# Performance work log

Hardware: AMD Instinct MI355X
Metric: run time of the kernel (lower is better)

## Reference

```python
import jax, jax.numpy as jnp
import numpy as np

N_NODES = 16384
IN_DIM = 256
HEADS = 2
OUT_CH = 256  # per head
SLOPE = 0.2


def _gat_conv(x, edge_index, W, att_src, att_dst, bias):
    """PyG GATConv (v1), heads=2, concat=True, add_self_loops=True."""
    N = x.shape[0]
    loop = jnp.arange(N)
    src = jnp.concatenate([edge_index[0], loop])  # message sources j
    dst = jnp.concatenate([edge_index[1], loop])  # message targets i
    h = (x @ W.T).reshape(N, HEADS, OUT_CH)          # [N,H,C]
    a_src = (h * att_src).sum(-1)                    # [N,H]
    a_dst = (h * att_dst).sum(-1)                    # [N,H]
    e = jax.nn.leaky_relu(a_src[src] + a_dst[dst], SLOPE)  # [E,H]
    # segment softmax over incoming edges of each dst node
    m = jax.ops.segment_max(e, dst, num_segments=N)
    e = jnp.exp(e - m[dst])
    s = jax.ops.segment_sum(e, dst, num_segments=N)
    alpha = e / s[dst]                               # [E,H]
    out = jax.ops.segment_sum(alpha[:, :, None] * h[src], dst, num_segments=N)
    return out.reshape(N, HEADS * OUT_CH) + bias


def _safe_cdist(x):
    sq = (x * x).sum(-1)
    d2 = sq[:, None] + sq[None, :] - 2.0 * (x @ x.T)
    d2 = jnp.maximum(d2, 0.0)
    d = jnp.sqrt(jnp.where(d2 > 0, d2, 1.0))
    return jnp.where(d2 > 0, d, 0.0)


def _linear_init(k, out_f, in_f):
    b = 1.0 / np.sqrt(in_f)
    k1, k2 = jax.random.split(k)
    W = jax.random.uniform(k1, (out_f, in_f), minval=-b, maxval=b, dtype=jnp.float32)
    bias = jax.random.uniform(k2, (out_f,), minval=-b, maxval=b, dtype=jnp.float32)
    return W, bias


def setup_inputs() -> dict:
    key = jax.random.key(0)
    ks = jax.random.split(key, 12)
    x = jax.random.normal(ks[0], (N_NODES, IN_DIM), dtype=jnp.float32)
    edge_index = jax.random.randint(ks[1], (2, 524288), 0, N_NODES, dtype=jnp.int64)
    g = 1.0 / np.sqrt(IN_DIM)
    conv_W = jax.random.normal(ks[2], (HEADS * OUT_CH, IN_DIM), dtype=jnp.float32) * g
    att_src = jax.random.normal(ks[3], (HEADS, OUT_CH), dtype=jnp.float32) * g
    att_dst = jax.random.normal(ks[4], (HEADS, OUT_CH), dtype=jnp.float32) * g
    conv_b = jnp.zeros((HEADS * OUT_CH,), dtype=jnp.float32)
    Wa, ba = _linear_init(ks[5], 256, 512)
    W1, b1 = _linear_init(ks[6], 128, 256)
    W2, b2 = _linear_init(ks[7], 64, 128)
    W3, b3 = _linear_init(ks[8], 32, 64)
    W4, b4 = _linear_init(ks[9], 3, 32)
    return {"x": x, "edge_index": edge_index, "conv_W": conv_W,
            "att_src": att_src, "att_dst": att_dst, "conv_b": conv_b,
            "Wa": Wa, "ba": ba, "W1": W1, "b1": b1, "W2": W2, "b2": b2,
            "W3": W3, "b3": b3, "W4": W4, "b4": b4}


def reference(x, edge_index, conv_W, att_src, att_dst, conv_b,
              Wa, ba, W1, b1, W2, b2, W3, b3, W4, b4):
    h = _gat_conv(x, edge_index, conv_W, att_src, att_dst, conv_b)
    h = jax.nn.relu(h)                      # dropout = identity (eval)
    h = jax.nn.relu(h @ Wa.T + ba)
    h = jax.nn.relu(h @ W1.T + b1)
    h = jax.nn.relu(h @ W2.T + b2)
    h = jax.nn.relu(h @ W3.T + b3)
    h = h @ W4.T + b4                        # [N,3]
    return _safe_cdist(h)                    # [N,N]
```

## Files before the change

kernel.cpp:

```cpp
#include <hip/hip_runtime.h>
#include <math.h>
#include <stdint.h>

#define N_NODES 16384
#define E_EDGES 524288
#define E_TOT   (E_EDGES + N_NODES)
#define HDIM    512
#define SLOPE   0.2f

typedef unsigned short ushort_t;
typedef __attribute__((ext_vector_type(8))) short short8v;
typedef __attribute__((ext_vector_type(4))) float f32x4;

__device__ __forceinline__ unsigned short f2bf(float f) {
    unsigned u = __float_as_uint(f);
    return (unsigned short)((u + 0x7fffu + ((u >> 16) & 1u)) >> 16);
}
__device__ __forceinline__ float bf2f(unsigned short s) {
    return __uint_as_float(((unsigned)s) << 16);
}

#define GLOAD_LDS16(G, L)                                                               \
    __builtin_amdgcn_global_load_lds((const __attribute__((address_space(1))) unsigned int*)(G), \
                                     (__attribute__((address_space(3))) unsigned int*)(L), 16, 0, 0)

__global__ void detect_kernel(const void* __restrict__ ei, int* __restrict__ flag) {
    int t = threadIdx.x;
    int v = ((const int*)ei)[2 * t + 1];
    unsigned long long b = __ballot(v != 0);
    if (t == 0) *flag = (b == 0ULL) ? 1 : 0;
}

__device__ __forceinline__ int edge_val(const void* ei, int idx, int is64) {
    if (is64) return (int)((const long long*)ei)[idx];
    return ((const int*)ei)[idx];
}

__global__ __launch_bounds__(256) void count_kernel(const void* __restrict__ ei,
                                                    const int* __restrict__ flag,
                                                    int* __restrict__ deg) {
    int e = blockIdx.x * 256 + threadIdx.x;
    if (e >= E_TOT) return;
    int is64 = *flag;
    int dst = (e < E_EDGES) ? edge_val(ei, E_EDGES + e, is64) : (e - E_EDGES);
    atomicAdd(&deg[dst], 1);
}

__global__ __launch_bounds__(1024) void scan_kernel(const int* __restrict__ deg,
                                                    int* __restrict__ rowptr,
                                                    int* __restrict__ cursor) {
    __shared__ int ps[1024];
    int tid = threadIdx.x;
    int base = tid * 16;
    int loc[16];
    int s = 0;
#pragma unroll
    for (int i = 0; i < 16; ++i) { loc[i] = deg[base + i]; s += loc[i]; }
    ps[tid] = s;
    __syncthreads();
    for (int off = 1; off < 1024; off <<= 1) {
        int t = (tid >= off) ? ps[tid - off] : 0;
        __syncthreads();
        if (tid >= off) ps[tid] += t;
        __syncthreads();
    }
    int run = ps[tid] - s;
#pragma unroll
    for (int i = 0; i < 16; ++i) {
        rowptr[base + i] = run;
        cursor[base + i] = run;
        run += loc[i];
    }
    if (tid == 1023) rowptr[N_NODES] = run;
}

__global__ __launch_bounds__(256) void fill_kernel(const void* __restrict__ ei,
                                                   const int* __restrict__ flag,
                                                   int* __restrict__ cursor,
                                                   int* __restrict__ col) {
    int e = blockIdx.x * 256 + threadIdx.x;
    if (e >= E_TOT) return;
    int is64 = *flag;
    int src, dst;
    if (e < E_EDGES) {
        src = edge_val(ei, e, is64);
        dst = edge_val(ei, E_EDGES + e, is64);
    } else {
        src = dst = e - E_EDGES;
    }
    int slot = atomicAdd(&cursor[dst], 1);
    col[slot] = src;
}

template <bool BSTYLE>
__global__ __launch_bounds__(256) void split3_kernel(const float* __restrict__ src,
                                                     ushort_t* __restrict__ dst,
                                                     int kshift) {
    int idx = (blockIdx.x * 256 + threadIdx.x) * 4;
    int K = 1 << kshift;
    int row = idx >> kshift, c = idx & (K - 1);
    float4 v = *(const float4*)&src[idx];
    float f[4] = {v.x, v.y, v.z, v.w};
    ushort_t h4[4], l4[4];
#pragma unroll
    for (int q = 0; q < 4; ++q) {
        ushort_t hb = f2bf(f[q]);
        float r = f[q] - bf2f(hb);
        h4[q] = hb;
        l4[q] = f2bf(r);
    }
    size_t b = (size_t)row * (3 * (size_t)K) + c;
    *(ushort4*)&dst[b] = make_ushort4(h4[0], h4[1], h4[2], h4[3]);
    size_t off_hi2 = BSTYLE ? (size_t)(2 * K) : (size_t)K;
    size_t off_lo  = BSTYLE ? (size_t)K : (size_t)(2 * K);
    *(ushort4*)&dst[b + off_hi2] = make_ushort4(h4[0], h4[1], h4[2], h4[3]);
    *(ushort4*)&dst[b + off_lo]  = make_ushort4(l4[0], l4[1], l4[2], l4[3]);
}

template <int BN, bool RELU, bool BIAS>
__global__ __launch_bounds__(256) void mfma_gemm(const ushort_t* __restrict__ A,
                                                 const ushort_t* __restrict__ B,
                                                 const float* __restrict__ bias,
                                                 float* __restrict__ C,
                                                 int M, int N, int K) {
    constexpr int BM = 128, BK = 64;
    constexpr int ASLOTS = BM * BK / (256 * 8);
    constexpr int BSLOTS = BN * BK / (256 * 8);
    constexpr int BNF = BN / 32;
    __shared__ ushort_t As[BM * BK];
    __shared__ ushort_t Bs[BN * BK];

    int t = threadIdx.x;
    int bm0 = blockIdx.y * BM, bn0 = blockIdx.x * BN;

    size_t gA[ASLOTS]; int lA[ASLOTS];
#pragma unroll
    for (int s = 0; s < ASLOTS; ++s) {
        int lin = s * 256 + t;
        int row = lin >> 3, cs = (lin & 7) << 3;
        int lcol = cs ^ ((row & 7) << 3);
        gA[s] = (size_t)(bm0 + row) * K + lcol;
        lA[s] = (s * 256 + (t & ~63)) * 8;
    }
    size_t gB[BSLOTS]; int lB[BSLOTS];
#pragma unroll
    for (int s = 0; s < BSLOTS; ++s) {
        int lin = s * 256 + t;
        int row = lin >> 3, cs = (lin & 7) << 3;
        int lcol = cs ^ ((row & 7) << 3);
        gB[s] = (size_t)(bn0 + row) * K + lcol;
        lB[s] = (s * 256 + (t & ~63)) * 8;
    }

    int l = t & 63, w = t >> 6;
    int wm = w >> 1, wn = w & 1;
    int lr = l & 15, lk = l >> 4;

    f32x4 acc[4][BNF];
#pragma unroll
    for (int m = 0; m < 4; ++m)
#pragma unroll
        for (int n = 0; n < BNF; ++n) acc[m][n] = (f32x4){0.f, 0.f, 0.f, 0.f};

    for (int k0 = 0; k0 < K; k0 += BK) {
#pragma unroll
        for (int s = 0; s < ASLOTS; ++s) GLOAD_LDS16(A + gA[s] + k0, As + lA[s]);
#pragma unroll
        for (int s = 0; s < BSLOTS; ++s) GLOAD_LDS16(B + gB[s] + k0, Bs + lB[s]);
        __syncthreads();
#pragma unroll
        for (int ks = 0; ks < 2; ++ks) {
            short8v af[4], bfr[BNF];
#pragma unroll
            for (int m = 0; m < 4; ++m) {
                int row = wm * 64 + m * 16 + lr;
                int c = (ks * 32 + lk * 8) ^ ((row & 7) << 3);
                af[m] = *(const short8v*)&As[row * 64 + c];
            }
#pragma unroll
            for (int n = 0; n < BNF; ++n) {
                int row = wn * (BN / 2) + n * 16 + lr;
                int c = (ks * 32 + lk * 8) ^ ((row & 7) << 3);
                bfr[n] = *(const short8v*)&Bs[row * 64 + c];
            }
#pragma unroll
            for (int m = 0; m < 4; ++m)
#pragma unroll
                for (int n = 0; n < BNF; ++n)
                    acc[m][n] = __builtin_amdgcn_mfma_f32_16x16x32_bf16(af[m], bfr[n],
                                                                        acc[m][n], 0, 0, 0);
        }
        __syncthreads();
    }

#pragma unroll
    for (int m = 0; m < 4; ++m) {
        int row0 = bm0 + wm * 64 + m * 16 + lk * 4;
#pragma unroll
        for (int n = 0; n < BNF; ++n) {
            int cix = bn0 + wn * (BN / 2) + n * 16 + lr;
            float bv = BIAS ? bias[cix] : 0.f;
#pragma unroll
            for (int r = 0; r < 4; ++r) {
                float v = acc[m][n][r] + bv;
                if (RELU) v = fmaxf(v, 0.f);
                C[(size_t)(row0 + r) * N + cix] = v;
            }
        }
    }
}

__global__ __launch_bounds__(256) void attn_kernel(const float* __restrict__ h,
                                                   const float* __restrict__ att_src,
                                                   const float* __restrict__ att_dst,
                                                   float* __restrict__ a_src,
                                                   float* __restrict__ a_dst) {
    int n = blockIdx.x, tid = threadIdx.x;
    float h0 = h[(size_t)n * HDIM + tid];
    float h1 = h[(size_t)n * HDIM + 256 + tid];
    __shared__ float4 red[256];
    red[tid] = make_float4(h0 * att_src[tid], h1 * att_src[256 + tid],
                           h0 * att_dst[tid], h1 * att_dst[256 + tid]);
    __syncthreads();
    for (int off = 128; off > 0; off >>= 1) {
        if (tid < off) {
            float4 o = red[tid + off];
            float4 m = red[tid];
            m.x += o.x; m.y += o.y; m.z += o.z; m.w += o.w;
            red[tid] = m;
        }
        __syncthreads();
    }
    if (tid == 0) {
        float4 r = red[0];
        a_src[2 * n] = r.x; a_src[2 * n + 1] = r.y;
        a_dst[2 * n] = r.z; a_dst[2 * n + 1] = r.w;
    }
}

__device__ __forceinline__ float lrelu(float x) {
    return fmaxf(x, 0.f) + SLOPE * fminf(x, 0.f);
}

__global__ __launch_bounds__(256) void aggregate_kernel(const float* __restrict__ h,
                                                        const float* __restrict__ a_src,
                                                        const float* __restrict__ a_dst,
                                                        const int* __restrict__ rowptr,
                                                        const int* __restrict__ col,
                                                        const float* __restrict__ conv_b,
                                                        float* __restrict__ act0) {
    int n = blockIdx.x, tid = threadIdx.x;
    int rs = rowptr[n], re = rowptr[n + 1];
    float ad0 = a_dst[2 * n], ad1 = a_dst[2 * n + 1];
    __shared__ float r0[256], r1[256];

    float m0 = -1e30f, m1 = -1e30f;
    for (int k = rs + tid; k < re; k += 256) {
        int s = col[k];
        float e0 = lrelu(a_src[2 * s] + ad0);
        float e1 = lrelu(a_src[2 * s + 1] + ad1);
        m0 = fmaxf(m0, e0); m1 = fmaxf(m1, e1);
    }
    r0[tid] = m0; r1[tid] = m1;
    __syncthreads();
    for (int off = 128; off > 0; off >>= 1) {
        if (tid < off) {
            r0[tid] = fmaxf(r0[tid], r0[tid + off]);
            r1[tid] = fmaxf(r1[tid], r1[tid + off]);
        }
        __syncthreads();
    }
    float M0 = r0[0], M1 = r1[0];
    __syncthreads();

    float s0 = 0.f, s1 = 0.f;
    for (int k = rs + tid; k < re; k += 256) {
        int s = col[k];
        float e0 = lrelu(a_src[2 * s] + ad0);
        float e1 = lrelu(a_src[2 * s + 1] + ad1);
        s0 += expf(e0 - M0); s1 += expf(e1 - M1);
    }
    r0[tid] = s0; r1[tid] = s1;
    __syncthreads();
    for (int off = 128; off > 0; off >>= 1) {
        if (tid < off) {
            r0[tid] += r0[tid + off];
            r1[tid] += r1[tid + off];
        }
        __syncthreads();
    }
    float inv0 = 1.f / r0[0], inv1 = 1.f / r1[0];
    __syncthreads();

    __shared__ float al0[256], al1[256];
    __shared__ int sc[256];
    float acc0 = 0.f, acc1 = 0.f;
    for (int base = rs; base < re; base += 256) {
        int len = min(256, re - base);
        if (tid < len) {
            int s = col[base + tid];
            sc[tid] = s;
            float e0 = lrelu(a_src[2 * s] + ad0);
            float e1 = lrelu(a_src[2 * s + 1] + ad1);
            al0[tid] = expf(e0 - M0) * inv0;
            al1[tid] = expf(e1 - M1) * inv1;
        }
        __syncthreads();
        for (int kk = 0; kk < len; ++kk) {
            const float* hr = h + (size_t)sc[kk] * HDIM;
            acc0 = fmaf(al0[kk], hr[tid], acc0);
            acc1 = fmaf(al1[kk], hr[tid + 256], acc1);
        }
        __syncthreads();
    }
    act0[(size_t)n * HDIM + tid] = fmaxf(acc0 + conv_b[tid], 0.f);
    act0[(size_t)n * HDIM + 256 + tid] = fmaxf(acc1 + conv_b[tid + 256], 0.f);
}

__global__ __launch_bounds__(256) void mlp_tail_kernel(const float* __restrict__ act2,
                                                       const float* __restrict__ W2, const float* __restrict__ b2,
                                                       const float* __restrict__ W3, const float* __restrict__ b3,
                                                       const float* __restrict__ W4, const float* __restrict__ b4,
                                                       float* __restrict__ p) {
    __shared__ float w2[64][129];
    __shared__ float w3[32][65];
    __shared__ float w4[3][33];
    __shared__ float bb2[64], bb3[32], bb4[3];
    __shared__ float xb[4][128];
    __shared__ float yb[4][64];
    __shared__ float zb[4][32];
    int tid = threadIdx.x;
    for (int idx = tid; idx < 64 * 128; idx += 256) w2[idx >> 7][idx & 127] = W2[idx];
    for (int idx = tid; idx < 32 * 64; idx += 256) w3[idx >> 6][idx & 63] = W3[idx];
    for (int idx = tid; idx < 96; idx += 256) w4[idx / 32][idx % 32] = W4[idx];
    if (tid < 64) bb2[tid] = b2[tid];
    if (tid < 32) bb3[tid] = b3[tid];
    if (tid < 3) bb4[tid] = b4[tid];
    __syncthreads();

    int n0 = blockIdx.x * 64;
    int nl = tid >> 6, lane = tid & 63;
    for (int g = 0; g < 64; g += 4) {
        for (int lx = tid; lx < 512; lx += 256)
            xb[lx >> 7][lx & 127] = act2[(size_t)(n0 + g + (lx >> 7)) * 128 + (lx & 127)];
        __syncthreads();
        float y = bb2[lane];
#pragma unroll 8
        for (int j = 0; j < 128; ++j) y = fmaf(w2[lane][j], xb[nl][j], y);
        yb[nl][lane] = fmaxf(y, 0.f);
        __syncthreads();
        if (lane < 32) {
            float z = bb3[lane];
#pragma unroll 8
            for (int j = 0; j < 64; ++j) z = fmaf(w3[lane][j], yb[nl][j], z);
            zb[nl][lane] = fmaxf(z, 0.f);
        }
        __syncthreads();
        if (lane < 3) {
            float c = bb4[lane];
#pragma unroll
            for (int j = 0; j < 32; ++j) c = fmaf(w4[lane][j], zb[nl][j], c);
            p[(size_t)(n0 + g + nl) * 3 + lane] = c;
        }
        __syncthreads();
    }
}

__global__ __launch_bounds__(256) void cdist_kernel(const float* __restrict__ p,
                                                    float* __restrict__ out) {
    int tid = threadIdx.x;
    int j0 = blockIdx.x * 1024 + tid * 4;
    int i0 = blockIdx.y * 64;
    __shared__ float pi[64][3];
    for (int lx = tid; lx < 192; lx += 256) pi[lx / 3][lx % 3] = p[i0 * 3 + lx];
    float px[4], py[4], pz[4];
#pragma unroll
    for (int q = 0; q < 4; ++q) {
        const float* pp = p + (size_t)(j0 + q) * 3;
        px[q] = pp[0]; py[q] = pp[1]; pz[q] = pp[2];
    }
    __syncthreads();
#pragma unroll 4
    for (int i = 0; i < 64; ++i) {
        float ax = pi[i][0], ay = pi[i][1], az = pi[i][2];
        float o[4];
#pragma unroll
        for (int q = 0; q < 4; ++q) {
            float dx = ax - px[q], dy = ay - py[q], dz = az - pz[q];
            float d2 = fmaf(dx, dx, fmaf(dy, dy, dz * dz));
            o[q] = (d2 > 0.f) ? sqrtf(d2) : 0.f;
        }
        *(float4*)(out + (size_t)(i0 + i) * N_NODES + j0) = make_float4(o[0], o[1], o[2], o[3]);
    }
}

extern "C" void kernel_launch(void* const* d_in, const int* in_sizes, int n_in,
                              void* d_out, int out_size, void* d_ws, size_t ws_size,
                              hipStream_t stream) {
    const float* x       = (const float*)d_in[0];
    const void*  ei      = d_in[1];
    const float* conv_W  = (const float*)d_in[2];
    const float* att_src = (const float*)d_in[3];
    const float* att_dst = (const float*)d_in[4];
    const float* conv_b  = (const float*)d_in[5];
    const float* Wa = (const float*)d_in[6];  const float* ba = (const float*)d_in[7];
    const float* W1 = (const float*)d_in[8];  const float* b1 = (const float*)d_in[9];
    const float* W2 = (const float*)d_in[10]; const float* b2 = (const float*)d_in[11];
    const float* W3 = (const float*)d_in[12]; const float* b3 = (const float*)d_in[13];
    const float* W4 = (const float*)d_in[14]; const float* b4 = (const float*)d_in[15];
    float* out = (float*)d_out;

    float* ws_f  = (float*)d_ws;
    float* h     = ws_f;
    float* act0  = h     + (size_t)N_NODES * HDIM;
    float* act1  = act0  + (size_t)N_NODES * HDIM;
    float* act2  = act1  + (size_t)N_NODES * 256;
    float* p3    = act2  + (size_t)N_NODES * 128;
    float* a_src = p3    + (size_t)N_NODES * 4;
    float* a_dst = a_src + N_NODES * 2;
    int* deg     = (int*)(a_dst + N_NODES * 2);
    int* rowptr  = deg + N_NODES;
    int* cursor  = rowptr + N_NODES + 1;
    int* colx    = cursor + N_NODES;
    int* flag    = colx + E_TOT;
    uintptr_t up = ((uintptr_t)(flag + 1) + 255) & ~(uintptr_t)255;
    ushort_t* x2  = (ushort_t*)up;
    ushort_t* a02 = x2  + (size_t)N_NODES * 768;
    ushort_t* a12 = a02 + (size_t)N_NODES * 1536;
    ushort_t* cw2 = a12 + (size_t)N_NODES * 768;
    ushort_t* wa2 = cw2 + (size_t)512 * 768;
    ushort_t* w12 = wa2 + (size_t)256 * 1536;

    hipMemsetAsync(deg, 0, N_NODES * sizeof(int), stream);
    detect_kernel<<<1, 64, 0, stream>>>(ei, flag);

    split3_kernel<false><<<N_NODES * 256 / 1024, 256, 0, stream>>>(x, x2, 8);
    split3_kernel<true><<<512 * 256 / 1024, 256, 0, stream>>>(conv_W, cw2, 8);
    split3_kernel<true><<<256 * 512 / 1024, 256, 0, stream>>>(Wa, wa2, 9);
    split3_kernel<true><<<128 * 256 / 1024, 256, 0, stream>>>(W1, w12, 8);

    mfma_gemm<128, false, false><<<dim3(4, 128), 256, 0, stream>>>(
        x2, cw2, nullptr, h, N_NODES, 512, 768);

    attn_kernel<<<N_NODES, 256, 0, stream>>>(h, att_src, att_dst, a_src, a_dst);

    count_kernel<<<E_TOT / 256, 256, 0, stream>>>(ei, flag, deg);
    scan_kernel<<<1, 1024, 0, stream>>>(deg, rowptr, cursor);
    fill_kernel<<<E_TOT / 256, 256, 0, stream>>>(ei, flag, cursor, colx);

    aggregate_kernel<<<N_NODES, 256, 0, stream>>>(h, a_src, a_dst, rowptr, colx,
                                                  conv_b, act0);

    split3_kernel<false><<<N_NODES * 512 / 1024, 256, 0, stream>>>(act0, a02, 9);
    mfma_gemm<128, true, true><<<dim3(2, 128), 256, 0, stream>>>(
        a02, wa2, ba, act1, N_NODES, 256, 1536);

    split3_kernel<false><<<N_NODES * 256 / 1024, 256, 0, stream>>>(act1, a12, 8);
    mfma_gemm<64, true, true><<<dim3(2, 128), 256, 0, stream>>>(
        a12, w12, b1, act2, N_NODES, 128, 768);

    mlp_tail_kernel<<<N_NODES / 64, 256, 0, stream>>>(act2, W2, b2, W3, b3, W4, b4, p3);

    cdist_kernel<<<dim3(16, 256), 256, 0, stream>>>(p3, out);
}
```

Before: 1.598 ms.

## Fuse bf16 split into aggregate and GEMM epilogues; wave-per-node aggregation

The GAT aggregation now runs one wavefront per destination node instead of one 256-thread block per node. It uses shuffle reductions, a single online pass that merges the exp-sum with the weighted gather, and float4 loads of the neighbour features. The aggregate kernel and the first MLP GEMM epilogue now write the hi/hi/lo bf16 split layout directly, which removes two split3 kernels and the fp32 act0/act1 round trips through memory. The trade-offs are uncoalesced 2-byte scalar stores in the GEMM epilogue and deferred normalization by the exp-sum.

```diff
diff --git a/kernel.cpp b/kernel.cpp
--- a/kernel.cpp
+++ b/kernel.cpp
@@ -117,11 +117,12 @@
     *(ushort4*)&dst[b + off_lo]  = make_ushort4(l4[0], l4[1], l4[2], l4[3]);
 }
 
-template <int BN, bool RELU, bool BIAS>
+template <int BN, int OUTMODE>
 __global__ __launch_bounds__(256) void mfma_gemm(const ushort_t* __restrict__ A,
                                                  const ushort_t* __restrict__ B,
                                                  const float* __restrict__ bias,
-                                                 float* __restrict__ C,
+                                                 float* __restrict__ Cf,
+                                                 ushort_t* __restrict__ Cs,
                                                  int M, int N, int K) {
     constexpr int BM = 128, BK = 64;
     constexpr int ASLOTS = BM * BK / (256 * 8);
@@ -199,12 +200,21 @@
 #pragma unroll
         for (int n = 0; n < BNF; ++n) {
             int cix = bn0 + wn * (BN / 2) + n * 16 + lr;
-            float bv = BIAS ? bias[cix] : 0.f;
+            float bv = (OUTMODE >= 1) ? bias[cix] : 0.f;
 #pragma unroll
             for (int r = 0; r < 4; ++r) {
                 float v = acc[m][n][r] + bv;
-                if (RELU) v = fmaxf(v, 0.f);
-                C[(size_t)(row0 + r) * N + cix] = v;
+                if (OUTMODE >= 1) v = fmaxf(v, 0.f);
+                if (OUTMODE == 2) {
+                    ushort_t hb = f2bf(v);
+                    ushort_t lb = f2bf(v - bf2f(hb));
+                    size_t rb = (size_t)(row0 + r) * (3 * (size_t)N);
+                    Cs[rb + cix] = hb;
+                    Cs[rb + N + cix] = hb;
+                    Cs[rb + 2 * N + cix] = lb;
+                } else {
+                    Cf[(size_t)(row0 + r) * N + cix] = v;
+                }
             }
         }
     }
@@ -248,73 +258,88 @@
                                                         const int* __restrict__ rowptr,
                                                         const int* __restrict__ col,
                                                         const float* __restrict__ conv_b,
-                                                        float* __restrict__ act0) {
-    int n = blockIdx.x, tid = threadIdx.x;
+                                                        ushort_t* __restrict__ a02) {
+    int n = (blockIdx.x * 256 + threadIdx.x) >> 6;
+    int lane = threadIdx.x & 63;
     int rs = rowptr[n], re = rowptr[n + 1];
     float ad0 = a_dst[2 * n], ad1 = a_dst[2 * n + 1];
-    __shared__ float r0[256], r1[256];
 
     float m0 = -1e30f, m1 = -1e30f;
-    for (int k = rs + tid; k < re; k += 256) {
+    for (int k = rs + lane; k < re; k += 64) {
         int s = col[k];
-        float e0 = lrelu(a_src[2 * s] + ad0);
-        float e1 = lrelu(a_src[2 * s + 1] + ad1);
-        m0 = fmaxf(m0, e0); m1 = fmaxf(m1, e1);
-    }
-    r0[tid] = m0; r1[tid] = m1;
-    __syncthreads();
-    for (int off = 128; off > 0; off >>= 1) {
-        if (tid < off) {
-            r0[tid] = fmaxf(r0[tid], r0[tid + off]);
-            r1[tid] = fmaxf(r1[tid], r1[tid + off]);
-        }
-        __syncthreads();
-    }
-    float M0 = r0[0], M1 = r1[0];
-    __syncthreads();
-
+        float2 av = *(const float2*)&a_src[2 * s];
+        m0 = fmaxf(m0, lrelu(av.x + ad0));
+        m1 = fmaxf(m1, lrelu(av.y + ad1));
+    }
+#pragma unroll
+    for (int off = 32; off > 0; off >>= 1) {
+        m0 = fmaxf(m0, __shfl_xor(m0, off));
+        m1 = fmaxf(m1, __shfl_xor(m1, off));
+    }
+
+    float4 acc0 = make_float4(0.f, 0.f, 0.f, 0.f);
+    float4 acc1 = make_float4(0.f, 0.f, 0.f, 0.f);
     float s0 = 0.f, s1 = 0.f;
-    for (int k = rs + tid; k < re; k += 256) {
-        int s = col[k];
-        float e0 = lrelu(a_src[2 * s] + ad0);
-        float e1 = lrelu(a_src[2 * s + 1] + ad1);
-        s0 += expf(e0 - M0); s1 += expf(e1 - M1);
-    }
-    r0[tid] = s0; r1[tid] = s1;
-    __syncthreads();
-    for (int off = 128; off > 0; off >>= 1) {
-        if (tid < off) {
-            r0[tid] += r0[tid + off];
-            r1[tid] += r1[tid + off];
-        }
-        __syncthreads();
-    }
-    float inv0 = 1.f / r0[0], inv1 = 1.f / r1[0];
-    __syncthreads();
-
-    __shared__ float al0[256], al1[256];
-    __shared__ int sc[256];
-    float acc0 = 0.f, acc1 = 0.f;
-    for (int base = rs; base < re; base += 256) {
-        int len = min(256, re - base);
-        if (tid < len) {
-            int s = col[base + tid];
-            sc[tid] = s;
-            float e0 = lrelu(a_src[2 * s] + ad0);
-            float e1 = lrelu(a_src[2 * s + 1] + ad1);
-            al0[tid] = expf(e0 - M0) * inv0;
-            al1[tid] = expf(e1 - M1) * inv1;
-        }
-        __syncthreads();
-        for (int kk = 0; kk < len; ++kk) {
-            const float* hr = h + (size_t)sc[kk] * HDIM;
-            acc0 = fmaf(al0[kk], hr[tid], acc0);
-            acc1 = fmaf(al1[kk], hr[tid + 256], acc1);
-        }
-        __syncthreads();
-    }
-    act0[(size_t)n * HDIM + tid] = fmaxf(acc0 + conv_b[tid], 0.f);
-    act0[(size_t)n * HDIM + 256 + tid] = fmaxf(acc1 + conv_b[tid + 256], 0.f);
+    for (int base = rs; base < re; base += 64) {
+        int k = base + lane;
+        int cnt = min(64, re - base);
+        float w0 = 0.f, w1 = 0.f;
+        int sv = 0;
+        if (k < re) {
+            sv = col[k];
+            float2 av = *(const float2*)&a_src[2 * sv];
+            w0 = expf(lrelu(av.x + ad0) - m0);
+            w1 = expf(lrelu(av.y + ad1) - m1);
+            s0 += w0; s1 += w1;
+        }
+#pragma unroll 4
+        for (int kk = 0; kk < cnt; ++kk) {
+            int sj = __shfl(sv, kk);
+            float w0j = __shfl(w0, kk);
+            float w1j = __shfl(w1, kk);
+            const float* hr = h + (size_t)sj * HDIM;
+            float4 hv0 = *(const float4*)&hr[lane * 4];
+            float4 hv1 = *(const float4*)&hr[256 + lane * 4];
+            acc0.x = fmaf(w0j, hv0.x, acc0.x);
+            acc0.y = fmaf(w0j, hv0.y, acc0.y);
+            acc0.z = fmaf(w0j, hv0.z, acc0.z);
+            acc0.w = fmaf(w0j, hv0.w, acc0.w);
+            acc1.x = fmaf(w1j, hv1.x, acc1.x);
+            acc1.y = fmaf(w1j, hv1.y, acc1.y);
+            acc1.z = fmaf(w1j, hv1.z, acc1.z);
+            acc1.w = fmaf(w1j, hv1.w, acc1.w);
+        }
+    }
+#pragma unroll
+    for (int off = 32; off > 0; off >>= 1) {
+        s0 += __shfl_xor(s0, off);
+        s1 += __shfl_xor(s1, off);
+    }
+    float i0 = 1.f / s0, i1 = 1.f / s1;
+
+    float4 b0 = *(const float4*)&conv_b[lane * 4];
+    float4 b1 = *(const float4*)&conv_b[256 + lane * 4];
+    float v0[4] = {fmaxf(acc0.x * i0 + b0.x, 0.f), fmaxf(acc0.y * i0 + b0.y, 0.f),
+                   fmaxf(acc0.z * i0 + b0.z, 0.f), fmaxf(acc0.w * i0 + b0.w, 0.f)};
+    float v1[4] = {fmaxf(acc1.x * i1 + b1.x, 0.f), fmaxf(acc1.y * i1 + b1.y, 0.f),
+                   fmaxf(acc1.z * i1 + b1.z, 0.f), fmaxf(acc1.w * i1 + b1.w, 0.f)};
+    ushort_t h0[4], l0[4], h1v[4], l1[4];
+#pragma unroll
+    for (int q = 0; q < 4; ++q) {
+        h0[q] = f2bf(v0[q]); l0[q] = f2bf(v0[q] - bf2f(h0[q]));
+        h1v[q] = f2bf(v1[q]); l1[q] = f2bf(v1[q] - bf2f(h1v[q]));
+    }
+    size_t rb = (size_t)n * 1536;
+    ushort4 uh0 = make_ushort4(h0[0], h0[1], h0[2], h0[3]);
+    ushort4 ul0 = make_ushort4(l0[0], l0[1], l0[2], l0[3]);
+    ushort4 uh1 = make_ushort4(h1v[0], h1v[1], h1v[2], h1v[3]);
+    ushort4 ul1 = make_ushort4(l1[0], l1[1], l1[2], l1[3]);
+    *(ushort4*)&a02[rb + lane * 4]        = uh0;
+    *(ushort4*)&a02[rb + 512 + lane * 4]  = uh0;
+    *(ushort4*)&a02[rb + 1024 + lane * 4] = ul0;
+    *(ushort4*)&a02[rb + 256 + lane * 4]  = uh1;
+    *(ushort4*)&a02[rb + 768 + lane * 4]  = uh1;
+    *(ushort4*)&a02[rb + 1280 + lane * 4] = ul1;
 }
 
 __global__ __launch_bounds__(256) void mlp_tail_kernel(const float* __restrict__ act2,
@@ -412,9 +437,7 @@
 
     float* ws_f  = (float*)d_ws;
     float* h     = ws_f;
-    float* act0  = h     + (size_t)N_NODES * HDIM;
-    float* act1  = act0  + (size_t)N_NODES * HDIM;
-    float* act2  = act1  + (size_t)N_NODES * 256;
+    float* act2  = h     + (size_t)N_NODES * HDIM;
     float* p3    = act2  + (size_t)N_NODES * 128;
     float* a_src = p3    + (size_t)N_NODES * 4;
     float* a_dst = a_src + N_NODES * 2;
@@ -439,8 +462,8 @@
     split3_kernel<true><<<256 * 512 / 1024, 256, 0, stream>>>(Wa, wa2, 9);
     split3_kernel<true><<<128 * 256 / 1024, 256, 0, stream>>>(W1, w12, 8);
 
-    mfma_gemm<128, false, false><<<dim3(4, 128), 256, 0, stream>>>(
-        x2, cw2, nullptr, h, N_NODES, 512, 768);
+    mfma_gemm<128, 0><<<dim3(4, 128), 256, 0, stream>>>(x2, cw2, nullptr, h, nullptr,
+                                                        N_NODES, 512, 768);
 
     attn_kernel<<<N_NODES, 256, 0, stream>>>(h, att_src, att_dst, a_src, a_dst);
 
@@ -448,16 +471,13 @@
     scan_kernel<<<1, 1024, 0, stream>>>(deg, rowptr, cursor);
     fill_kernel<<<E_TOT / 256, 256, 0, stream>>>(ei, flag, cursor, colx);
 
-    aggregate_kernel<<<N_NODES, 256, 0, stream>>>(h, a_src, a_dst, rowptr, colx,
-                                                  conv_b, act0);
-
-    split3_kernel<false><<<N_NODES * 512 / 1024, 256, 0, stream>>>(act0, a02, 9);
-    mfma_gemm<128, true, true><<<dim3(2, 128), 256, 0, stream>>>(
-        a02, wa2, ba, act1, N_NODES, 256, 1536);
-
-    split3_kernel<false><<<N_NODES * 256 / 1024, 256, 0, stream>>>(act1, a12, 8);
-    mfma_gemm<64, true, true><<<dim3(2, 128), 256, 0, stream>>>(
-        a12, w12, b1, act2, N_NODES, 128, 768);
+    aggregate_kernel<<<N_NODES / 4, 256, 0, stream>>>(h, a_src, a_dst, rowptr, colx,
+                                                      conv_b, a02);
+
+    mfma_gemm<128, 2><<<dim3(2, 128), 256, 0, stream>>>(a02, wa2, ba, nullptr, a12,
+                                                        N_NODES, 256, 1536);
+    mfma_gemm<64, 1><<<dim3(2, 128), 256, 0, stream>>>(a12, w12, b1, act2, nullptr,
+                                                       N_NODES, 128, 768);
 
     mlp_tail_kernel<<<N_NODES / 64, 256, 0, stream>>>(act2, W2, b2, W3, b3, W4, b4, p3);
 
```

New measurement: 1.584 ms. About the same (-0.9%).
